# Optimization experiments

Hardware: AMD Instinct MI355X
Metric: run time of the kernel (lower is better)

## Reference

```python
import jax, jax.numpy as jnp
import numpy as np

HEADS = 24
HEAD_DIM = 128
DIM = HEADS * HEAD_DIM  # 3072
EPS = 1e-6


def setup_inputs() -> dict:
    key = jax.random.key(0)
    ks = jax.random.split(key, 10)
    B, S_IMG, S_TXT = 1, 2048, 256
    hidden_states = jax.random.normal(ks[0], (B, S_IMG, DIM), jnp.float32)
    encoder_hidden_states = jax.random.normal(ks[1], (B, S_TXT, DIM), jnp.float32)
    # RoPE tables for image tokens, interleaved pair layout [S_IMG, HEAD_DIM]
    inv = 1.0 / (10000.0 ** (np.arange(0, HEAD_DIM, 2, dtype=np.float32) / HEAD_DIM))
    ang = np.arange(S_IMG, dtype=np.float32)[:, None] * inv[None, :]  # [S, Dh/2]
    ang = np.repeat(ang, 2, axis=-1)  # [S, Dh], pairs (2i, 2i+1) share angle
    rope_cos = jnp.asarray(np.cos(ang), jnp.float32)
    rope_sin = jnp.asarray(np.sin(ang), jnp.float32)
    s = 0.02
    wq = jax.random.normal(ks[2], (DIM, DIM), jnp.float32) * s
    wk = jax.random.normal(ks[3], (DIM, DIM), jnp.float32) * s
    wv = jax.random.normal(ks[4], (DIM, DIM), jnp.float32) * s
    wo = jax.random.normal(ks[5], (DIM, DIM), jnp.float32) * s
    bq = jax.random.normal(ks[6], (DIM,), jnp.float32) * s
    bk = jax.random.normal(ks[7], (DIM,), jnp.float32) * s
    bv = jax.random.normal(ks[8], (DIM,), jnp.float32) * s
    bo = jax.random.normal(ks[9], (DIM,), jnp.float32) * s
    norm_q_w = jnp.ones((HEAD_DIM,), jnp.float32)
    norm_k_w = jnp.ones((HEAD_DIM,), jnp.float32)
    return dict(hidden_states=hidden_states, encoder_hidden_states=encoder_hidden_states,
                rope_cos=rope_cos, rope_sin=rope_sin,
                wq=wq, bq=bq, wk=wk, bk=bk, wv=wv, bv=bv,
                norm_q_w=norm_q_w, norm_k_w=norm_k_w, wo=wo, bo=bo)


def _rmsnorm(x, w):
    var = jnp.mean(jnp.square(x), axis=-1, keepdims=True)
    return x * jax.lax.rsqrt(var + EPS) * w


def _rope(x, cos, sin):
    # x [B,H,S,Dh]; diffusers apply_rotary_emb with use_real_unbind_dim=-1:
    # pairs are interleaved (x[2i], x[2i+1]) -> rotated = stack(-imag, real)
    xr = x[..., 0::2]
    xi = x[..., 1::2]
    x_rot = jnp.stack([-xi, xr], axis=-1).reshape(x.shape)
    return x * cos + x_rot * sin


def reference(hidden_states, encoder_hidden_states, rope_cos, rope_sin,
              wq, bq, wk, bk, wv, bv, norm_q_w, norm_k_w, wo, bo):
    B, s_img, D = hidden_states.shape
    s_txt = encoder_hidden_states.shape[1]
    S = s_img + s_txt
    x = jnp.concatenate([hidden_states, encoder_hidden_states], axis=1)  # [B,S,D]

    def proj(w, b):
        return (x @ w + b).reshape(B, S, HEADS, HEAD_DIM).transpose(0, 2, 1, 3)  # [B,H,S,Dh]

    q = _rmsnorm(proj(wq, bq), norm_q_w)
    k = _rmsnorm(proj(wk, bk), norm_k_w)
    v = proj(wv, bv)
    # RoPE on image tokens only
    q = jnp.concatenate([_rope(q[:, :, :s_img], rope_cos, rope_sin), q[:, :, s_img:]], axis=2)
    k = jnp.concatenate([_rope(k[:, :, :s_img], rope_cos, rope_sin), k[:, :, s_img:]], axis=2)
    scale = 1.0 / jnp.sqrt(jnp.float32(HEAD_DIM))
    scores = jnp.einsum('bhqd,bhkd->bhqk', q, k) * scale
    attn = jax.nn.softmax(scores, axis=-1)
    out = jnp.einsum('bhqk,bhkd->bhqd', attn, v)
    out = out.transpose(0, 2, 1, 3).reshape(B, S, D)
    img = out[:, :s_img] @ wo + bo  # to_out[0]; to_out[1] is Dropout(p=0) -> identity
    txt = out[:, s_img:]            # to_add_out is None in this branch
    return img, txt
```

## Files before the change

### kernel.cpp

```cpp
#include <hip/hip_runtime.h>
#include <cstdint>

typedef __bf16 bf16_t;
typedef bf16_t bf16x8 __attribute__((ext_vector_type(8)));
typedef bf16_t bf16x4 __attribute__((ext_vector_type(4)));
typedef float  floatx4 __attribute__((ext_vector_type(4)));

#define S_ALL 2304
#define SIMG  2048
#define NH    24
#define HD    128
#define DIM   3072
#define NQKV  9216

#define SHIFT2 17.312340490667562f
#define QSCALE 0.12751744f

typedef __attribute__((address_space(1))) void* gp1_t;
typedef __attribute__((address_space(3))) void* lp3_t;

__device__ __forceinline__ void async16(const void* g, void* l) {
    __builtin_amdgcn_global_load_lds((gp1_t)(g), (lp3_t)(l), 16, 0, 0);
}
__device__ __forceinline__ floatx4 mfma_bf16(bf16x8 a, bf16x8 b, floatx4 c) {
    return __builtin_amdgcn_mfma_f32_16x16x32_bf16(a, b, c, 0, 0, 0);
}
__device__ __forceinline__ void barrier_raw() {
    asm volatile("s_barrier" ::: "memory");
}

__global__ __launch_bounds__(256) void k_convert_x(const float* __restrict__ hid,
                                                   const float* __restrict__ enc,
                                                   bf16_t* __restrict__ xb) {
    long i = ((long)blockIdx.x * 256 + threadIdx.x) * 4;
    const long HN = (long)SIMG * DIM;
    float4 f = (i < HN) ? *(const float4*)(hid + i) : *(const float4*)(enc + (i - HN));
    bf16x4 o;
    o[0] = (bf16_t)f.x; o[1] = (bf16_t)f.y; o[2] = (bf16_t)f.z; o[3] = (bf16_t)f.w;
    *(bf16x4*)(xb + i) = o;
}

__global__ __launch_bounds__(256) void k_wT4(const float* __restrict__ wq, const float* __restrict__ wk,
                                             const float* __restrict__ wv, const float* __restrict__ wo,
                                             bf16_t* __restrict__ wTq, bf16_t* __restrict__ woT) {
    __shared__ __align__(16) bf16_t T[64][72];
    int z = blockIdx.z;
    const float* W = (z == 0) ? wq : (z == 1) ? wk : (z == 2) ? wv : wo;
    bf16_t* Wt = (z < 3) ? (wTq + (long)z * DIM * DIM) : woT;
    int r0 = blockIdx.x * 64, c0 = blockIdx.y * 64;
    int tid = threadIdx.x;
    int lr = tid >> 2, lc = (tid & 3) * 16;
    const float* src = W + (long)(r0 + lr) * DIM + c0 + lc;
#pragma unroll
    for (int i = 0; i < 16; i += 4) {
        float4 f = *(const float4*)(src + i);
        T[lr][lc + i + 0] = (bf16_t)f.x;
        T[lr][lc + i + 1] = (bf16_t)f.y;
        T[lr][lc + i + 2] = (bf16_t)f.z;
        T[lr][lc + i + 3] = (bf16_t)f.w;
    }
    __syncthreads();
    bf16x8 a, b;
#pragma unroll
    for (int i = 0; i < 8; i++) a[i] = T[lc + i][lr];
#pragma unroll
    for (int i = 0; i < 8; i++) b[i] = T[lc + 8 + i][lr];
    bf16_t* dst = Wt + (long)(c0 + lr) * DIM + r0 + lc;
    *(bf16x8*)dst = a;
    *(bf16x8*)(dst + 8) = b;
}

__device__ __forceinline__ void gemm_pipe_256x256(const bf16_t* __restrict__ A,
                                                  const bf16_t* __restrict__ Bt,
                                                  long m0, long n0, const int K,
                                                  char* smem, int tid,
                                                  floatx4 acc[8][4]) {
    const int wave = tid >> 6, lane = tid & 63;
    const int quad = lane >> 4, l16 = lane & 15;
    const int wm = (wave >> 2) * 128;
    const int wn = (wave & 3) * 64;
    const int kxor = ((lane & 7) ^ ((lane >> 3) & 7)) * 8;
    const bf16_t* Ag = A + (m0 + wave * 32 + (lane >> 3)) * K + kxor;
    const bf16_t* Bg = Bt + (n0 + wave * 32 + (lane >> 3)) * K + kxor;
    char* Asl = smem + wave * 4096;
    char* Bsl = smem + 65536 + wave * 4096;

    const int NT = K >> 6;

#pragma unroll
    for (int c2 = 0; c2 < 4; ++c2) async16(Ag + (long)c2 * 8 * K, Asl + c2 * 1024);
#pragma unroll
    for (int c2 = 0; c2 < 4; ++c2) async16(Bg + (long)c2 * 8 * K, Bsl + c2 * 1024);
    asm volatile("s_waitcnt vmcnt(0)" ::: "memory");
    barrier_raw();

    for (int kt = 0; kt < NT; ++kt) {
        const int cur = kt & 1;
        const bf16_t* As = (const bf16_t*)(smem + cur * 32768);
        const bf16_t* Bs = (const bf16_t*)(smem + 65536 + cur * 32768);

        if (kt + 1 < NT) {
            const long kg = (long)(kt + 1) * 64;
            char* Asd = Asl + (cur ^ 1) * 32768;
            char* Bsd = Bsl + (cur ^ 1) * 32768;
#pragma unroll
            for (int c2 = 0; c2 < 4; ++c2) async16(Ag + (long)c2 * 8 * K + kg, Asd + c2 * 1024);
#pragma unroll
            for (int c2 = 0; c2 < 4; ++c2) async16(Bg + (long)c2 * 8 * K + kg, Bsd + c2 * 1024);
        }

#pragma unroll
        for (int ks = 0; ks < 2; ++ks) {
            const int ch = ((ks * 4 + quad) ^ (l16 & 7)) * 8;
            bf16x8 bfr[4];
#pragma unroll
            for (int j = 0; j < 4; j++) bfr[j] = *(const bf16x8*)&Bs[(wn + j * 16 + l16) * 64 + ch];
#pragma unroll
            for (int g = 0; g < 2; ++g) {
                bf16x8 af[4];
#pragma unroll
                for (int i = 0; i < 4; i++)
                    af[i] = *(const bf16x8*)&As[(wm + (g * 4 + i) * 16 + l16) * 64 + ch];
                __builtin_amdgcn_s_setprio(1);
#pragma unroll
                for (int i = 0; i < 4; i++)
#pragma unroll
                    for (int j = 0; j < 4; j++)
                        acc[g * 4 + i][j] = mfma_bf16(af[i], bfr[j], acc[g * 4 + i][j]);
                __builtin_amdgcn_s_setprio(0);
            }
        }

        asm volatile("s_waitcnt vmcnt(0)" ::: "memory");
        barrier_raw();
    }
}

__global__ __launch_bounds__(512, 2) void k_gemm_qkv(const bf16_t* __restrict__ A,
                                                     const bf16_t* __restrict__ Bt,
                                                     const float* __restrict__ bq_,
                                                     const float* __restrict__ bk_,
                                                     const float* __restrict__ bv_,
                                                     const float* __restrict__ rope_cos,
                                                     const float* __restrict__ rope_sin,
                                                     const float* __restrict__ nqw,
                                                     const float* __restrict__ nkw,
                                                     bf16_t* __restrict__ qo,
                                                     bf16_t* __restrict__ ko,
                                                     bf16_t* __restrict__ vT) {
    __shared__ __align__(16) char smem[131072];
    int tid = threadIdx.x;
    int wave = tid >> 6, lane = tid & 63;
    int quad = lane >> 4, l16 = lane & 15;
    int x_n = blockIdx.x, y_m = blockIdx.y;
    long m0 = (long)y_m * 256, n0 = (long)x_n * 256;
    int t = x_n / 12, hb = (x_n % 12) * 2;
    int wm = (wave >> 2) * 128, wn = (wave & 3) * 64;
    int h2w = (wave & 3) >> 1;
    int halfw = wave & 1;

    floatx4 zero = {0.f, 0.f, 0.f, 0.f};
    floatx4 acc[8][4];
#pragma unroll
    for (int i = 0; i < 8; i++)
#pragma unroll
        for (int j = 0; j < 4; j++) acc[i][j] = zero;

    gemm_pipe_256x256(A, Bt, m0, n0, DIM, smem, tid, acc);

    int dcol[4];
#pragma unroll
    for (int j = 0; j < 4; j++) dcol[j] = halfw * 64 + j * 16 + l16;

    if (t == 2) {
        char* vbuf = smem;
#pragma unroll
        for (int h2 = 0; h2 < 2; ++h2)
#pragma unroll
            for (int rh = 0; rh < 2; ++rh) {
                if ((wave >> 2) == rh && h2w == h2) {
                    float bias4[4];
#pragma unroll
                    for (int j = 0; j < 4; j++) bias4[j] = bv_[(hb + h2) * HD + dcol[j]];
#pragma unroll
                    for (int i = 0; i < 8; i++)
#pragma unroll
                        for (int r = 0; r < 4; r++) {
                            int s_l = i * 16 + quad * 4 + r;
#pragma unroll
                            for (int j = 0; j < 4; j++) {
                                int d = dcol[j];
                                int chunk = d * 16 + ((s_l >> 3) ^ (d & 15));
                                *(bf16_t*)(vbuf + chunk * 16 + (s_l & 7) * 2) =
                                    (bf16_t)(acc[i][j][r] + bias4[j]);
                            }
                        }
                }
                __syncthreads();
                int d = tid >> 2, sh = tid & 3;
                bf16_t* dstv = vT + (long)(hb + h2) * HD * S_ALL + (long)d * S_ALL
                             + m0 + rh * 128 + sh * 32;
#pragma unroll
                for (int k8 = 0; k8 < 4; ++k8) {
                    int s8 = sh * 4 + k8;
                    bf16x8 frag = *(const bf16x8*)(vbuf + (d * 16 + (s8 ^ (d & 15))) * 16);
                    *(bf16x8*)(dstv + k8 * 8) = frag;
                }
                __syncthreads();
            }
    } else {
        float* ssq = (float*)smem;
        const float* bp = t ? bk_ : bq_;
        const float* nw = t ? nkw : nqw;
        int h = hb + h2w;
        float bias4[4], wv4[4];
#pragma unroll
        for (int j = 0; j < 4; j++) {
            bias4[j] = bp[h * HD + dcol[j]];
            wv4[j] = nw[dcol[j]];
        }
#pragma unroll
        for (int i = 0; i < 8; i++)
#pragma unroll
            for (int r = 0; r < 4; r++) {
                int row = wm + i * 16 + quad * 4 + r;
                float s2 = 0.f;
#pragma unroll
                for (int j = 0; j < 4; j++) {
                    float v = acc[i][j][r] + bias4[j];
                    acc[i][j][r] = v;
                    s2 += v * v;
                }
                s2 += __shfl_xor(s2, 1);
                s2 += __shfl_xor(s2, 2);
                s2 += __shfl_xor(s2, 4);
                s2 += __shfl_xor(s2, 8);
                if (l16 == 0) ssq[(h2w * 256 + row) * 2 + halfw] = s2;
            }
        __syncthreads();
        bf16_t* dst = (t ? ko : qo) + (long)h * S_ALL * HD;
        bool do_rope = (m0 < SIMG);
#pragma unroll
        for (int i = 0; i < 8; i++)
#pragma unroll
            for (int r = 0; r < 4; r++) {
                int row = wm + i * 16 + quad * 4 + r;
                int s_abs = (int)m0 + row;
                float tot = ssq[(h2w * 256 + row) * 2] + ssq[(h2w * 256 + row) * 2 + 1];
                float rms = rsqrtf(tot * (1.0f / 128.0f) + 1e-6f);
                float y[4];
#pragma unroll
                for (int j = 0; j < 4; j++) y[j] = acc[i][j][r] * rms * wv4[j];
                if (do_rope) {
                    const float* cp = rope_cos + (long)s_abs * HD;
                    const float* sp = rope_sin + (long)s_abs * HD;
#pragma unroll
                    for (int j = 0; j < 4; j++) {
                        float c = cp[dcol[j]], sn = sp[dcol[j]];
                        float px = __shfl_xor(y[j], 1);
                        y[j] = y[j] * c + ((l16 & 1) ? px : -px) * sn;
                    }
                }
#pragma unroll
                for (int j = 0; j < 4; j++) {
                    float v = t ? y[j] : y[j] * QSCALE;
                    dst[(long)s_abs * HD + dcol[j]] = (bf16_t)v;
                }
            }
    }
}

__global__ __launch_bounds__(512, 2) void k_gemm_bt(const bf16_t* __restrict__ A,
                                                    const bf16_t* __restrict__ Bt,
                                                    const float* __restrict__ bias,
                                                    bf16_t* __restrict__ Cb, float* __restrict__ Cf,
                                                    int M, int N, int K) {
    __shared__ __align__(16) char smem[131072];
    int tid = threadIdx.x;
    int wave = tid >> 6, lane = tid & 63;
    int quad = lane >> 4, l16 = lane & 15;
    long m0 = (long)blockIdx.y * 256, n0 = (long)blockIdx.x * 256;
    int wm = (wave >> 2) * 128, wn = (wave & 3) * 64;

    floatx4 zero = {0.f, 0.f, 0.f, 0.f};
    floatx4 acc[8][4];
#pragma unroll
    for (int i = 0; i < 8; i++)
#pragma unroll
        for (int j = 0; j < 4; j++) acc[i][j] = zero;

    gemm_pipe_256x256(A, Bt, m0, n0, K, smem, tid, acc);

#pragma unroll
    for (int i = 0; i < 8; i++) {
        long rowb = m0 + wm + i * 16 + quad * 4;
#pragma unroll
        for (int j = 0; j < 4; j++) {
            long col = n0 + wn + j * 16 + l16;
            float bv = bias ? bias[col] : 0.0f;
#pragma unroll
            for (int r = 0; r < 4; r++) {
                float v = acc[i][j][r] + bv;
                long idx = (rowb + r) * N + col;
                if (Cb) Cb[idx] = (bf16_t)v;
                else    Cf[idx] = v;
            }
        }
    }
}

__global__ __launch_bounds__(256, 2) void k_attn(const bf16_t* __restrict__ q,
                                                 const bf16_t* __restrict__ k,
                                                 const bf16_t* __restrict__ vT,
                                                 bf16_t* __restrict__ ao,
                                                 float* __restrict__ out_txt) {
    __shared__ __align__(16) bf16_t Ks[64 * 128];
    __shared__ __align__(16) bf16_t VTs[128 * 64];
    __shared__ __align__(16) bf16_t Ps[4][2][16 * 64];
    int tid = threadIdx.x, wave = tid >> 6, lane = tid & 63;
    int quad = lane >> 4, l16 = lane & 15;
    int h = blockIdx.y;
    int q0 = blockIdx.x * 128 + wave * 32;
    const long hbase = (long)h * S_ALL * HD;
    const char* kgb = (const char*)(k + hbase);
    const char* vgb = (const char*)(vT + hbase);

    int koffB[4], voffB[4], slotB[4];
#pragma unroll
    for (int c2 = 0; c2 < 4; ++c2) {
        int L = (wave * 4 + c2) * 64 + lane;
        slotB[c2] = L;
        int rk = L >> 4, ck = (L & 15) ^ (rk & 15);
        koffB[c2] = rk * 256 + ck * 16;
        int rv = L >> 3, cv = (L & 7) ^ (rv & 7) ^ (((rv >> 3) & 1) << 2);
        voffB[c2] = rv * (S_ALL * 2) + cv * 16;
    }

    bf16x8 qf[2][4];
#pragma unroll
    for (int st = 0; st < 2; ++st) {
        const bf16_t* qp = q + hbase + (long)(q0 + st * 16 + l16) * HD + quad * 8;
#pragma unroll
        for (int ks = 0; ks < 4; ++ks) qf[st][ks] = *(const bf16x8*)(qp + ks * 32);
    }

    floatx4 zero = {0.f, 0.f, 0.f, 0.f};
    floatx4 o0[8], o1[8];
#pragma unroll
    for (int ni = 0; ni < 8; ++ni) { o0[ni] = zero; o1[ni] = zero; }
    floatx4 lac0 = zero, lac1 = zero;

    for (int kb = 0; kb < S_ALL / 64; ++kb) {
        const char* kg = kgb + (long)kb * 16384;
        const char* vg = vgb + kb * 128;
#pragma unroll
        for (int c2 = 0; c2 < 4; ++c2) {
            async16(kg + koffB[c2], (char*)Ks + slotB[c2] * 16);
            async16(vg + voffB[c2], (char*)VTs + slotB[c2] * 16);
        }
        __syncthreads();

        floatx4 s0[4], s1[4];
#pragma unroll
        for (int ni = 0; ni < 4; ++ni) { s0[ni] = zero; s1[ni] = zero; }
#pragma unroll
        for (int ks = 0; ks < 4; ++ks)
#pragma unroll
            for (int ni = 0; ni < 4; ++ni) {
                int slot = (ni * 16 + l16) * 16 + ((ks * 4 + quad) ^ l16);
                bf16x8 kf = *(const bf16x8*)&Ks[slot * 8];
                s0[ni] = mfma_bf16(qf[0][ks], kf, s0[ni]);
                s1[ni] = mfma_bf16(qf[1][ks], kf, s1[ni]);
            }

#pragma unroll
        for (int st = 0; st < 2; ++st) {
#pragma unroll
            for (int ni = 0; ni < 4; ++ni) {
                floatx4 sv = st ? s1[ni] : s0[ni];
                floatx4 p;
#pragma unroll
                for (int j = 0; j < 4; ++j) p[j] = __builtin_amdgcn_exp2f(sv[j] - SHIFT2);
                if (st) lac1 += p; else lac0 += p;
#pragma unroll
                for (int j = 0; j < 4; ++j) {
                    int r = quad * 4 + j;
                    int chunk = ((ni * 16 + l16) >> 3) ^ ((r >> 1) & 7);
                    Ps[wave][st][r * 64 + chunk * 8 + (l16 & 7)] = (bf16_t)p[j];
                }
            }
        }

        bf16x8 pf[2][2];
#pragma unroll
        for (int st = 0; st < 2; ++st)
#pragma unroll
            for (int k2 = 0; k2 < 2; ++k2) {
                int chunk = (k2 * 4 + quad) ^ ((l16 >> 1) & 7);
                pf[st][k2] = *(const bf16x8*)&Ps[wave][st][l16 * 64 + chunk * 8];
            }

#pragma unroll
        for (int k2 = 0; k2 < 2; ++k2)
#pragma unroll
            for (int ni = 0; ni < 8; ++ni) {
                int r = ni * 16 + l16;
                int c = (k2 * 4 + quad) ^ (l16 & 7) ^ (((l16 >> 3) & 1) << 2);
                bf16x8 vf = *(const bf16x8*)&VTs[r * 64 + c * 8];
                o0[ni] = mfma_bf16(pf[0][k2], vf, o0[ni]);
                o1[ni] = mfma_bf16(pf[1][k2], vf, o1[ni]);
            }
        __syncthreads();
    }

#pragma unroll
    for (int off = 1; off < 16; off <<= 1) {
#pragma unroll
        for (int j = 0; j < 4; ++j) {
            lac0[j] += __shfl_xor(lac0[j], off);
            lac1[j] += __shfl_xor(lac1[j], off);
        }
    }

#pragma unroll
    for (int st = 0; st < 2; ++st) {
#pragma unroll
        for (int j = 0; j < 4; ++j) {
            float rl = 1.0f / (st ? lac1[j] : lac0[j]);
            int s_row = q0 + st * 16 + quad * 4 + j;
#pragma unroll
            for (int ni = 0; ni < 8; ++ni) {
                float v = (st ? o1[ni][j] : o0[ni][j]) * rl;
                int col = h * HD + ni * 16 + l16;
                ao[(long)s_row * DIM + col] = (bf16_t)v;
                if (s_row >= SIMG) out_txt[(long)(s_row - SIMG) * DIM + col] = v;
            }
        }
    }
}

extern "C" void kernel_launch(void* const* d_in, const int* in_sizes, int n_in,
                              void* d_out, int out_size, void* d_ws, size_t ws_size,
                              hipStream_t stream) {
    const float* hid = (const float*)d_in[0];
    const float* enc = (const float*)d_in[1];
    const float* rope_cos = (const float*)d_in[2];
    const float* rope_sin = (const float*)d_in[3];
    const float* wq = (const float*)d_in[4];
    const float* bq = (const float*)d_in[5];
    const float* wk = (const float*)d_in[6];
    const float* bk = (const float*)d_in[7];
    const float* wv = (const float*)d_in[8];
    const float* bv = (const float*)d_in[9];
    const float* nqw = (const float*)d_in[10];
    const float* nkw = (const float*)d_in[11];
    const float* wo = (const float*)d_in[12];
    const float* bo = (const float*)d_in[13];
    float* out = (float*)d_out;

    char* ws = (char*)d_ws;
    bf16_t* xb   = (bf16_t*)(ws);
    bf16_t* wTq  = (bf16_t*)(ws + 14155776L);
    bf16_t* woT  = (bf16_t*)(ws + 70778880L);
    bf16_t* qb   = (bf16_t*)(ws + 89653248L);
    bf16_t* kbuf = (bf16_t*)(ws + 103809024L);
    bf16_t* vT   = (bf16_t*)(ws + 117964800L);
    bf16_t* ao   = (bf16_t*)(ws + 132120576L);

    k_convert_x<<<6912, 256, 0, stream>>>(hid, enc, xb);
    k_wT4<<<dim3(48, 48, 4), 256, 0, stream>>>(wq, wk, wv, wo, wTq, woT);
    k_gemm_qkv<<<dim3(36, 9), 512, 0, stream>>>(xb, wTq, bq, bk, bv, rope_cos, rope_sin,
                                                nqw, nkw, qb, kbuf, vT);
    k_attn<<<dim3(18, 24), 256, 0, stream>>>(qb, kbuf, vT, ao, out + (long)SIMG * DIM);
    k_gemm_bt<<<dim3(12, 8), 512, 0, stream>>>(ao, woT, bo, (bf16_t*)nullptr, out, SIMG, DIM, DIM);
}
```

Measured before the change: 576.3 us.

## Rework GEMM pipeline to 4-slot K32 staging with retiled QKV and output grids

```diff
diff --git a/kernel.cpp b/kernel.cpp
--- a/kernel.cpp
+++ b/kernel.cpp
@@ -27,6 +27,15 @@
 }
 __device__ __forceinline__ void barrier_raw() {
     asm volatile("s_barrier" ::: "memory");
+}
+template<int N> __device__ __forceinline__ void s_vmcnt() {
+    if constexpr (N == 0)      asm volatile("s_waitcnt vmcnt(0)" ::: "memory");
+    else if constexpr (N == 6) asm volatile("s_waitcnt vmcnt(6)" ::: "memory");
+    else if constexpr (N == 8) asm volatile("s_waitcnt vmcnt(8)" ::: "memory");
+}
+template<int VH, int VL> __device__ __forceinline__ void vmcnt_w(int wave) {
+    if constexpr (VH == VL) s_vmcnt<VH>();
+    else { if (wave < 4) s_vmcnt<VH>(); else s_vmcnt<VL>(); }
 }
 
 __global__ __launch_bounds__(256) void k_convert_x(const float* __restrict__ hid,
@@ -70,69 +79,83 @@
     *(bf16x8*)(dst + 8) = b;
 }
 
-__device__ __forceinline__ void gemm_pipe_256x256(const bf16_t* __restrict__ A,
-                                                  const bf16_t* __restrict__ Bt,
-                                                  long m0, long n0, const int K,
-                                                  char* smem, int tid,
-                                                  floatx4 acc[8][4]) {
+template<int BM, int BN, int NWN, int AF, int VH, int VL>
+__device__ __forceinline__ void gemm_pipe_s32(const bf16_t* __restrict__ A,
+                                              const bf16_t* __restrict__ Bt,
+                                              long m0, long n0, const int K,
+                                              char* smem, int tid,
+                                              floatx4 (&acc)[AF][4]) {
+    constexpr int SLOTB = (BM + BN) * 64;
+    constexpr int AH = AF / 2;
     const int wave = tid >> 6, lane = tid & 63;
     const int quad = lane >> 4, l16 = lane & 15;
-    const int wm = (wave >> 2) * 128;
-    const int wn = (wave & 3) * 64;
-    const int kxor = ((lane & 7) ^ ((lane >> 3) & 7)) * 8;
-    const bf16_t* Ag = A + (m0 + wave * 32 + (lane >> 3)) * K + kxor;
-    const bf16_t* Bg = Bt + (n0 + wave * 32 + (lane >> 3)) * K + kxor;
-    char* Asl = smem + wave * 4096;
-    char* Bsl = smem + 65536 + wave * 4096;
-
-    const int NT = K >> 6;
-
-#pragma unroll
-    for (int c2 = 0; c2 < 4; ++c2) async16(Ag + (long)c2 * 8 * K, Asl + c2 * 1024);
-#pragma unroll
-    for (int c2 = 0; c2 < 4; ++c2) async16(Bg + (long)c2 * 8 * K, Bsl + c2 * 1024);
-    asm volatile("s_waitcnt vmcnt(0)" ::: "memory");
+    const int wm = (wave / NWN) * (AF * 16);
+    const int wn = (wave % NWN) * 64;
+    const int rsw = ((l16 >> 1) & 3) << 4;
+    const int kc = ((lane & 3) ^ ((lane >> 3) & 3)) * 8;
+    const bf16_t* Ag = A + (m0 + (lane >> 2)) * K + kc;
+    const bf16_t* Bg = Bt + (n0 + (lane >> 2)) * K + kc;
+
+    auto stageA = [&](int s) {
+        char* base = smem + (s & 3) * SLOTB;
+        const bf16_t* g = Ag + s * 32;
+#pragma unroll
+        for (int r0 = 0; r0 < BM; r0 += 128)
+            if (BM - r0 >= 128 || wave * 16 < BM - r0)
+                async16(g + (long)(r0 + wave * 16) * K, base + r0 * 64 + wave * 1024);
+    };
+    auto stageB = [&](int s) {
+        char* base = smem + (s & 3) * SLOTB + BM * 64;
+        const bf16_t* g = Bg + s * 32;
+#pragma unroll
+        for (int r0 = 0; r0 < BN; r0 += 128)
+            if (BN - r0 >= 128 || wave * 16 < BN - r0)
+                async16(g + (long)(r0 + wave * 16) * K, base + r0 * 64 + wave * 1024);
+    };
+
+    const int NS = K >> 5;
+
+    stageA(0); stageB(0);
+    stageA(1); stageB(1);
+    stageA(2); stageB(2);
+    vmcnt_w<VH, VL>(wave);
     barrier_raw();
 
-    for (int kt = 0; kt < NT; ++kt) {
-        const int cur = kt & 1;
-        const bf16_t* As = (const bf16_t*)(smem + cur * 32768);
-        const bf16_t* Bs = (const bf16_t*)(smem + 65536 + cur * 32768);
-
-        if (kt + 1 < NT) {
-            const long kg = (long)(kt + 1) * 64;
-            char* Asd = Asl + (cur ^ 1) * 32768;
-            char* Bsd = Bsl + (cur ^ 1) * 32768;
-#pragma unroll
-            for (int c2 = 0; c2 < 4; ++c2) async16(Ag + (long)c2 * 8 * K + kg, Asd + c2 * 1024);
-#pragma unroll
-            for (int c2 = 0; c2 < 4; ++c2) async16(Bg + (long)c2 * 8 * K + kg, Bsd + c2 * 1024);
-        }
-
-#pragma unroll
-        for (int ks = 0; ks < 2; ++ks) {
-            const int ch = ((ks * 4 + quad) ^ (l16 & 7)) * 8;
-            bf16x8 bfr[4];
-#pragma unroll
-            for (int j = 0; j < 4; j++) bfr[j] = *(const bf16x8*)&Bs[(wn + j * 16 + l16) * 64 + ch];
-#pragma unroll
-            for (int g = 0; g < 2; ++g) {
-                bf16x8 af[4];
-#pragma unroll
-                for (int i = 0; i < 4; i++)
-                    af[i] = *(const bf16x8*)&As[(wm + (g * 4 + i) * 16 + l16) * 64 + ch];
-                __builtin_amdgcn_s_setprio(1);
-#pragma unroll
-                for (int i = 0; i < 4; i++)
-#pragma unroll
-                    for (int j = 0; j < 4; j++)
-                        acc[g * 4 + i][j] = mfma_bf16(af[i], bfr[j], acc[g * 4 + i][j]);
-                __builtin_amdgcn_s_setprio(0);
-            }
-        }
-
-        asm volatile("s_waitcnt vmcnt(0)" ::: "memory");
+    for (int s = 0; s < NS; ++s) {
+        const char* sA = smem + (s & 3) * SLOTB;
+        const char* sB = sA + BM * 64;
+        const bool stg = (s < NS - 3);
+
+        if (stg) stageA(s + 3);
+        bf16x8 a0[AH], b0[4];
+#pragma unroll
+        for (int i = 0; i < AH; ++i)
+            a0[i] = *(const bf16x8*)(sA + (wm + i * 16 + l16) * 64 + ((quad << 4) ^ rsw));
+#pragma unroll
+        for (int j = 0; j < 4; ++j)
+            b0[j] = *(const bf16x8*)(sB + (wn + j * 16 + l16) * 64 + ((quad << 4) ^ rsw));
         barrier_raw();
+        __builtin_amdgcn_s_setprio(1);
+#pragma unroll
+        for (int i = 0; i < AH; ++i)
+#pragma unroll
+            for (int j = 0; j < 4; ++j) acc[i][j] = mfma_bf16(a0[i], b0[j], acc[i][j]);
+        __builtin_amdgcn_s_setprio(0);
+
+        if (stg) stageB(s + 3);
+        bf16x8 a1[AF - AH];
+#pragma unroll
+        for (int i = AH; i < AF; ++i)
+            a1[i - AH] = *(const bf16x8*)(sA + (wm + i * 16 + l16) * 64 + ((quad << 4) ^ rsw));
+        if (stg) vmcnt_w<VH, VL>(wave);
+        else     s_vmcnt<0>();
+        barrier_raw();
+        __builtin_amdgcn_s_setprio(1);
+#pragma unroll
+        for (int i = AH; i < AF; ++i)
+#pragma unroll
+            for (int j = 0; j < 4; ++j) acc[i][j] = mfma_bf16(a1[i - AH], b0[j], acc[i][j]);
+        __builtin_amdgcn_s_setprio(0);
     }
 }
 
@@ -148,25 +171,24 @@
                                                      bf16_t* __restrict__ qo,
                                                      bf16_t* __restrict__ ko,
                                                      bf16_t* __restrict__ vT) {
-    __shared__ __align__(16) char smem[131072];
+    __shared__ __align__(16) char smem[114688];
     int tid = threadIdx.x;
     int wave = tid >> 6, lane = tid & 63;
     int quad = lane >> 4, l16 = lane & 15;
-    int x_n = blockIdx.x, y_m = blockIdx.y;
-    long m0 = (long)y_m * 256, n0 = (long)x_n * 256;
-    int t = x_n / 12, hb = (x_n % 12) * 2;
-    int wm = (wave >> 2) * 128, wn = (wave & 3) * 64;
+    long m0 = (long)blockIdx.y * 192, n0 = (long)blockIdx.x * 256;
+    int t = blockIdx.x / 12, hb = (blockIdx.x % 12) * 2;
+    int wm = (wave >> 2) * 96;
     int h2w = (wave & 3) >> 1;
     int halfw = wave & 1;
 
     floatx4 zero = {0.f, 0.f, 0.f, 0.f};
-    floatx4 acc[8][4];
-#pragma unroll
-    for (int i = 0; i < 8; i++)
+    floatx4 acc[6][4];
+#pragma unroll
+    for (int i = 0; i < 6; i++)
 #pragma unroll
         for (int j = 0; j < 4; j++) acc[i][j] = zero;
 
-    gemm_pipe_256x256(A, Bt, m0, n0, DIM, smem, tid, acc);
+    gemm_pipe_s32<192, 256, 4, 6, 8, 6>(A, Bt, m0, n0, DIM, smem, tid, acc);
 
     int dcol[4];
 #pragma unroll
@@ -175,39 +197,43 @@
     if (t == 2) {
         char* vbuf = smem;
 #pragma unroll
-        for (int h2 = 0; h2 < 2; ++h2)
-#pragma unroll
-            for (int rh = 0; rh < 2; ++rh) {
-                if ((wave >> 2) == rh && h2w == h2) {
+        for (int h2 = 0; h2 < 2; ++h2) {
+#pragma unroll
+            for (int g3 = 0; g3 < 3; ++g3) {
+                if (h2w == h2) {
                     float bias4[4];
 #pragma unroll
                     for (int j = 0; j < 4; j++) bias4[j] = bv_[(hb + h2) * HD + dcol[j]];
 #pragma unroll
-                    for (int i = 0; i < 8; i++)
-#pragma unroll
-                        for (int r = 0; r < 4; r++) {
-                            int s_l = i * 16 + quad * 4 + r;
-#pragma unroll
-                            for (int j = 0; j < 4; j++) {
-                                int d = dcol[j];
-                                int chunk = d * 16 + ((s_l >> 3) ^ (d & 15));
-                                *(bf16_t*)(vbuf + chunk * 16 + (s_l & 7) * 2) =
-                                    (bf16_t)(acc[i][j][r] + bias4[j]);
+                    for (int i = 0; i < 6; i++) {
+                        if (((wm + i * 16) >> 6) == g3) {
+#pragma unroll
+                            for (int r = 0; r < 4; r++) {
+                                int s_l = wm + i * 16 + quad * 4 + r - g3 * 64;
+#pragma unroll
+                                for (int j = 0; j < 4; j++) {
+                                    int d = dcol[j];
+                                    int chunk = d * 8 + ((s_l >> 3) ^ (d & 7));
+                                    *(bf16_t*)(vbuf + chunk * 16 + (s_l & 7) * 2) =
+                                        (bf16_t)(acc[i][j][r] + bias4[j]);
+                                }
                             }
                         }
+                    }
                 }
                 __syncthreads();
                 int d = tid >> 2, sh = tid & 3;
                 bf16_t* dstv = vT + (long)(hb + h2) * HD * S_ALL + (long)d * S_ALL
-                             + m0 + rh * 128 + sh * 32;
-#pragma unroll
-                for (int k8 = 0; k8 < 4; ++k8) {
-                    int s8 = sh * 4 + k8;
-                    bf16x8 frag = *(const bf16x8*)(vbuf + (d * 16 + (s8 ^ (d & 15))) * 16);
-                    *(bf16x8*)(dstv + k8 * 8) = frag;
+                             + m0 + g3 * 64;
+#pragma unroll
+                for (int u = 0; u < 2; ++u) {
+                    int s8 = sh * 2 + u;
+                    bf16x8 frag = *(const bf16x8*)(vbuf + (d * 8 + (s8 ^ (d & 7))) * 16);
+                    *(bf16x8*)(dstv + s8 * 8) = frag;
                 }
                 __syncthreads();
             }
+        }
     } else {
         float* ssq = (float*)smem;
         const float* bp = t ? bk_ : bq_;
@@ -220,7 +246,7 @@
             wv4[j] = nw[dcol[j]];
         }
 #pragma unroll
-        for (int i = 0; i < 8; i++)
+        for (int i = 0; i < 6; i++)
 #pragma unroll
             for (int r = 0; r < 4; r++) {
                 int row = wm + i * 16 + quad * 4 + r;
@@ -235,23 +261,22 @@
                 s2 += __shfl_xor(s2, 2);
                 s2 += __shfl_xor(s2, 4);
                 s2 += __shfl_xor(s2, 8);
-                if (l16 == 0) ssq[(h2w * 256 + row) * 2 + halfw] = s2;
+                if (l16 == 0) ssq[(h2w * 192 + row) * 2 + halfw] = s2;
             }
         __syncthreads();
         bf16_t* dst = (t ? ko : qo) + (long)h * S_ALL * HD;
-        bool do_rope = (m0 < SIMG);
-#pragma unroll
-        for (int i = 0; i < 8; i++)
+#pragma unroll
+        for (int i = 0; i < 6; i++)
 #pragma unroll
             for (int r = 0; r < 4; r++) {
                 int row = wm + i * 16 + quad * 4 + r;
                 int s_abs = (int)m0 + row;
-                float tot = ssq[(h2w * 256 + row) * 2] + ssq[(h2w * 256 + row) * 2 + 1];
+                float tot = ssq[(h2w * 192 + row) * 2] + ssq[(h2w * 192 + row) * 2 + 1];
                 float rms = rsqrtf(tot * (1.0f / 128.0f) + 1e-6f);
                 float y[4];
 #pragma unroll
                 for (int j = 0; j < 4; j++) y[j] = acc[i][j][r] * rms * wv4[j];
-                if (do_rope) {
+                if (s_abs < SIMG) {
                     const float* cp = rope_cos + (long)s_abs * HD;
                     const float* sp = rope_sin + (long)s_abs * HD;
 #pragma unroll
@@ -275,24 +300,24 @@
                                                     const float* __restrict__ bias,
                                                     bf16_t* __restrict__ Cb, float* __restrict__ Cf,
                                                     int M, int N, int K) {
-    __shared__ __align__(16) char smem[131072];
+    __shared__ __align__(16) char smem[98304];
     int tid = threadIdx.x;
     int wave = tid >> 6, lane = tid & 63;
     int quad = lane >> 4, l16 = lane & 15;
-    long m0 = (long)blockIdx.y * 256, n0 = (long)blockIdx.x * 256;
-    int wm = (wave >> 2) * 128, wn = (wave & 3) * 64;
+    long m0 = (long)blockIdx.y * 256, n0 = (long)blockIdx.x * 128;
+    int wm = (wave >> 1) * 64, wn = (wave & 1) * 64;
 
     floatx4 zero = {0.f, 0.f, 0.f, 0.f};
-    floatx4 acc[8][4];
-#pragma unroll
-    for (int i = 0; i < 8; i++)
+    floatx4 acc[4][4];
+#pragma unroll
+    for (int i = 0; i < 4; i++)
 #pragma unroll
         for (int j = 0; j < 4; j++) acc[i][j] = zero;
 
-    gemm_pipe_256x256(A, Bt, m0, n0, K, smem, tid, acc);
-
-#pragma unroll
-    for (int i = 0; i < 8; i++) {
+    gemm_pipe_s32<256, 128, 2, 4, 6, 6>(A, Bt, m0, n0, K, smem, tid, acc);
+
+#pragma unroll
+    for (int i = 0; i < 4; i++) {
         long rowb = m0 + wm + i * 16 + quad * 4;
 #pragma unroll
         for (int j = 0; j < 4; j++) {
@@ -469,8 +494,8 @@
 
     k_convert_x<<<6912, 256, 0, stream>>>(hid, enc, xb);
     k_wT4<<<dim3(48, 48, 4), 256, 0, stream>>>(wq, wk, wv, wo, wTq, woT);
-    k_gemm_qkv<<<dim3(36, 9), 512, 0, stream>>>(xb, wTq, bq, bk, bv, rope_cos, rope_sin,
-                                                nqw, nkw, qb, kbuf, vT);
+    k_gemm_qkv<<<dim3(36, 12), 512, 0, stream>>>(xb, wTq, bq, bk, bv, rope_cos, rope_sin,
+                                                 nqw, nkw, qb, kbuf, vT);
     k_attn<<<dim3(18, 24), 256, 0, stream>>>(qb, kbuf, vT, ao, out + (long)SIMG * DIM);
-    k_gemm_bt<<<dim3(12, 8), 512, 0, stream>>>(ao, woT, bo, (bf16_t*)nullptr, out, SIMG, DIM, DIM);
-}
+    k_gemm_bt<<<dim3(24, 8), 512, 0, stream>>>(ao, woT, bo, (bf16_t*)nullptr, out, SIMG, DIM, DIM);
+}
```

New measurement: 541.6 us. -6.0%, faster.
